# Optimization experiments

Measured on AMD Instinct MI355X. Metric: run time of the kernel, lower is better.

The kernel has to match this reference:

```python
import jax, jax.numpy as jnp
import numpy as np

B, S, D = 2, 2048, 4096
N_Q_HEADS, N_KV_HEADS, HEAD_DIM = 32, 8, 128
N_REP = N_Q_HEADS // N_KV_HEADS
ROPE_THETA = 10000.0


def setup_inputs() -> dict:
    key = jax.random.key(0)
    ks = jax.random.split(key, 5)
    x = jax.random.normal(ks[0], (B, S, D), dtype=jnp.float32)
    sc = 1.0 / np.sqrt(D)
    wq = jax.random.normal(ks[1], (D, N_Q_HEADS * HEAD_DIM), dtype=jnp.float32) * sc
    wk = jax.random.normal(ks[2], (D, N_KV_HEADS * HEAD_DIM), dtype=jnp.float32) * sc
    wv = jax.random.normal(ks[3], (D, N_KV_HEADS * HEAD_DIM), dtype=jnp.float32) * sc
    cache_k = jnp.zeros((B, S, N_KV_HEADS, HEAD_DIM), dtype=jnp.float32)
    cache_v = jnp.zeros((B, S, N_KV_HEADS, HEAD_DIM), dtype=jnp.float32)
    # rotary frequencies: theta_i = 1/ROPE_THETA^(2i/hd), angle = pos * theta_i
    inv_freq = 1.0 / (ROPE_THETA ** (np.arange(0, HEAD_DIM, 2, dtype=np.float32) / HEAD_DIM))
    angles = np.arange(S, dtype=np.float32)[:, None] * inv_freq[None, :]  # [S, hd/2]
    freqs_cos = jnp.asarray(np.cos(angles), dtype=jnp.float32)
    freqs_sin = jnp.asarray(np.sin(angles), dtype=jnp.float32)
    return {"x": x, "wq": wq, "wk": wk, "wv": wv,
            "cache_k": cache_k, "cache_v": cache_v,
            "freqs_cos": freqs_cos, "freqs_sin": freqs_sin,
            "start_pos": 0}


def _apply_rope(x, cos, sin):
    # x: [B, S, H, hd]; cos/sin: [S, hd/2] -> complex rotation of adjacent pairs
    xr = x[..., 0::2]
    xi = x[..., 1::2]
    c = cos[None, :, None, :]
    s = sin[None, :, None, :]
    out_r = xr * c - xi * s
    out_i = xr * s + xi * c
    return jnp.stack([out_r, out_i], axis=-1).reshape(x.shape)


def reference(x, wq, wk, wv, cache_k, cache_v, freqs_cos, freqs_sin, start_pos):
    batch, seq_len, _ = x.shape
    xq = (x @ wq).reshape(batch, seq_len, N_Q_HEADS, HEAD_DIM)
    xk = (x @ wk).reshape(batch, seq_len, N_KV_HEADS, HEAD_DIM)
    xv = (x @ wv).reshape(batch, seq_len, N_KV_HEADS, HEAD_DIM)
    xq = _apply_rope(xq, freqs_cos, freqs_sin)
    xk = _apply_rope(xk, freqs_cos, freqs_sin)
    # KV-cache append
    cache_k = jax.lax.dynamic_update_slice(cache_k, xk, (0, start_pos, 0, 0))
    cache_v = jax.lax.dynamic_update_slice(cache_v, xv, (0, start_pos, 0, 0))
    keys = cache_k[:, : start_pos + seq_len]    # [B, T, Hkv, hd]
    values = cache_v[:, : start_pos + seq_len]
    # GQA: repeat kv heads to match query heads
    keys = jnp.repeat(keys, N_REP, axis=2)      # [B, T, Hq, hd]
    values = jnp.repeat(values, N_REP, axis=2)
    scale = 1.0 / jnp.sqrt(jnp.asarray(HEAD_DIM, dtype=x.dtype))
    scores = jnp.einsum("bqhd,bkhd->bhqk", xq, keys) * scale
    probs = jax.nn.softmax(scores.astype(jnp.float32), axis=-1).astype(xq.dtype)
    out = jnp.einsum("bhqk,bkhd->bqhd", probs, values)
    return out.reshape(batch, seq_len, N_Q_HEADS * HEAD_DIM)
```

## Files before the change

### kernel.cpp

```cpp
#include <hip/hip_runtime.h>

#define BATCH   2
#define S_LEN   2048
#define D_MODEL 4096
#define HD      128
#define NQH     32
#define NKVH    8

typedef unsigned short ushort_t;
typedef __bf16 bf16x8 __attribute__((ext_vector_type(8)));
typedef float floatx4 __attribute__((ext_vector_type(4)));

#define MFMA16(a, b, c) __builtin_amdgcn_mfma_f32_16x16x32_bf16(a, b, c, 0, 0, 0)

#if __has_builtin(__builtin_amdgcn_exp2f)
#define EXP2(x) __builtin_amdgcn_exp2f(x)
#else
#define EXP2(x) __expf((x) * 0.6931471805599453f)
#endif

__device__ __forceinline__ ushort_t f2b(float f) {
    unsigned int x;
    __builtin_memcpy(&x, &f, 4);
    x += 0x7fff + ((x >> 16) & 1);
    return (ushort_t)(x >> 16);
}

__device__ __forceinline__ void gld16(void* lds, const void* g) {
    __builtin_amdgcn_global_load_lds(
        (const __attribute__((address_space(1))) void*)g,
        (__attribute__((address_space(3))) void*)lds, 16, 0, 0);
}

__global__ __launch_bounds__(256) void conv_x(const float* __restrict__ x,
                                              ushort_t* __restrict__ x0,
                                              ushort_t* __restrict__ x1) {
    const size_t i = ((size_t)blockIdx.x * 256 + threadIdx.x) << 2;
    float4 v = *(const float4*)&x[i];
    ushort4 p;
    p.x = f2b(v.x); p.y = f2b(v.y); p.z = f2b(v.z); p.w = f2b(v.w);
    ushort_t* dst = (i < 8388608) ? x0 : x1;
    *(ushort4*)&dst[i & 8388607] = p;
}

__global__ __launch_bounds__(256) void pack_w(const float* __restrict__ wq,
                                              const float* __restrict__ wk,
                                              const float* __restrict__ wv,
                                              ushort_t* __restrict__ WT) {
    __shared__ ushort_t t[64][65];
    const int k0 = blockIdx.x << 6;
    const int n0 = blockIdx.y << 6;
    const float* src;
    int scol, sN;
    if (n0 < 4096)      { src = wq; scol = n0;        sN = 4096; }
    else if (n0 < 5120) { src = wk; scol = n0 - 4096; sN = 1024; }
    else                { src = wv; scol = n0 - 5120; sN = 1024; }
    const int tid = threadIdx.x;
#pragma unroll
    for (int i = 0; i < 16; i++) {
        int idx = tid + (i << 8);
        int r = idx >> 6, c = idx & 63;
        t[r][c] = f2b(src[(size_t)(k0 + r) * sN + scol + c]);
    }
    __syncthreads();
#pragma unroll
    for (int i = 0; i < 16; i++) {
        int idx = tid + (i << 8);
        int r = idx >> 6, c = idx & 63;
        WT[(size_t)(n0 + r) * D_MODEL + k0 + c] = t[c][r];
    }
}

__global__ __launch_bounds__(256) void gemm_qkv(const ushort_t* __restrict__ x0,
                                                const ushort_t* __restrict__ x1,
                                                const ushort_t* __restrict__ WT,
                                                const float* __restrict__ fc,
                                                const float* __restrict__ fs,
                                                ushort_t* __restrict__ Qr,
                                                ushort_t* __restrict__ Kr,
                                                ushort_t* __restrict__ Vt) {
    __shared__ ushort_t At[128 * 64];
    __shared__ ushort_t Bt[128 * 64];
    const int tid  = threadIdx.x;
    const int wid  = tid >> 6;
    const int lane = tid & 63;
    const int bm = blockIdx.y << 7;
    const int bn = blockIdx.x << 7;
    const int wm = (wid & 1) << 6;
    const int wn = (wid >> 1) << 6;

    floatx4 acc[4][4] = {};

    const ushort_t* Xb = (bm < 2048) ? x0 : x1;
    const int bml = bm & 2047;

    const int g = (lane & 7) ^ (lane >> 3);
    const ushort_t* gA = Xb + (size_t)(bml + (wid << 5) + (lane >> 3)) * D_MODEL + (g << 3);
    const ushort_t* gB = WT + (size_t)(bn  + (wid << 5) + (lane >> 3)) * D_MODEL + (g << 3);
    ushort_t* lA = &At[wid << 11];
    ushort_t* lB = &Bt[wid << 11];
    const int l7 = lane & 7;
    const int cl = lane & 15, rg = lane >> 4;

    for (int k0 = 0; k0 < D_MODEL; k0 += 64) {
        __syncthreads();
#pragma unroll
        for (int i = 0; i < 4; i++) {
            gld16(lA + (i << 9), gA + (size_t)(i << 3) * D_MODEL + k0);
            gld16(lB + (i << 9), gB + (size_t)(i << 3) * D_MODEL + k0);
        }
        __syncthreads();
#pragma unroll
        for (int kk = 0; kk < 2; kk++) {
            const int c = (kk << 2) + rg;
            const int slot = (c ^ l7) << 3;
            bf16x8 af[4], bfr[4];
#pragma unroll
            for (int mm = 0; mm < 4; mm++) {
                af[mm]  = *(const bf16x8*)&At[((wm + (mm << 4) + cl) << 6) + slot];
                bfr[mm] = *(const bf16x8*)&Bt[((wn + (mm << 4) + cl) << 6) + slot];
            }
#pragma unroll
            for (int mm = 0; mm < 4; mm++)
#pragma unroll
                for (int nn = 0; nn < 4; nn++)
                    acc[mm][nn] = MFMA16(af[mm], bfr[nn], acc[mm][nn]);
        }
    }

    const int region = blockIdx.x;
    const int b_idx  = bm >> 11;
    const int s0w    = (bm & 2047) + wm;

    if (region < 40) {
        const float oscale = (region < 32)
            ? (0.08838834764831845f * 1.4426950408889634f) : 1.0f;
        ushort_t* dst;
        if (region < 32) dst = Qr + (size_t)(b_idx * NQH  +  region      ) * S_LEN * HD;
        else             dst = Kr + (size_t)(b_idx * NKVH + (region - 32)) * S_LEN * HD;
#pragma unroll
        for (int nn = 0; nn < 4; nn++) {
            const int dcol = wn + (nn << 4) + cl;
            const int d2   = dcol >> 1;
            const float sgn = (dcol & 1) ? 1.0f : -1.0f;
#pragma unroll
            for (int mm = 0; mm < 4; mm++)
#pragma unroll
                for (int r = 0; r < 4; r++) {
                    float v  = acc[mm][nn][r];
                    float pv = __shfl_xor(v, 1);
                    int srow = s0w + (mm << 4) + (rg << 2) + r;
                    float c  = fc[(srow << 6) + d2];
                    float s  = fs[(srow << 6) + d2];
                    float o  = (v * c + sgn * pv * s) * oscale;
                    dst[(size_t)srow * HD + dcol] = f2b(o);
                }
        }
    } else {
        const int kvh = region - 40;
        ushort_t* dst = Vt + (size_t)(b_idx * NKVH + kvh) * HD * S_LEN;
#pragma unroll
        for (int mm = 0; mm < 4; mm++) {
            const int srow = s0w + (mm << 4) + (rg << 2);
#pragma unroll
            for (int nn = 0; nn < 4; nn++) {
                const int dcol = wn + (nn << 4) + cl;
                ushort4 pk;
                pk.x = f2b(acc[mm][nn][0]);
                pk.y = f2b(acc[mm][nn][1]);
                pk.z = f2b(acc[mm][nn][2]);
                pk.w = f2b(acc[mm][nn][3]);
                *(ushort4*)&dst[(size_t)dcol * S_LEN + srow] = pk;
            }
        }
    }
}

__global__ __launch_bounds__(256, 3) void attn(const ushort_t* __restrict__ Qr,
                                               const ushort_t* __restrict__ Kr,
                                               const ushort_t* __restrict__ Vtg,
                                               float* __restrict__ out) {
    __shared__ ushort_t Kt[64 * 128];
    __shared__ ushort_t Vl[128 * 64];
    __shared__ ushort_t Pt[4 * 32 * 68];

    const int tid  = threadIdx.x;
    const int wid  = tid >> 6;
    const int lane = tid & 63;
    const int h  = blockIdx.y;
    const int b  = blockIdx.z;
    const int kh = h >> 2;
    const int q0 = (blockIdx.x << 7) + (wid << 5);

    const int cl = lane & 15, rg = lane >> 4, l7 = lane & 7;

    const ushort_t* Qbase = Qr + ((size_t)(b * NQH + h) * S_LEN + q0 + cl) * HD;
    bf16x8 qf0[4], qf1[4];
#pragma unroll
    for (int dc = 0; dc < 4; dc++) {
        qf0[dc] = *(const bf16x8*)&Qbase[(dc << 5) + (rg << 3)];
        qf1[dc] = *(const bf16x8*)&Qbase[(size_t)16 * HD + (dc << 5) + (rg << 3)];
    }

    floatx4 o0[8] = {}, o1[8] = {};
    float ls0[4] = {0.f, 0.f, 0.f, 0.f};
    float ls1[4] = {0.f, 0.f, 0.f, 0.f};

    const ushort_t* Kb = Kr  + (size_t)(b * NKVH + kh) * S_LEN * HD;
    const ushort_t* Vb = Vtg + (size_t)(b * NKVH + kh) * HD * S_LEN;
    ushort_t* Pw = &Pt[wid * 32 * 68];
    const int gv = (lane & 7) ^ (lane >> 3);

    for (int kt0 = 0; kt0 < S_LEN; kt0 += 64) {
        __syncthreads();
#pragma unroll
        for (int i = 0; i < 4; i++) {
            int issue = (wid << 2) + i;
            int gk = cl ^ (((i & 1) << 2) + rg);
            gld16(&Kt[issue << 9],
                  Kb + (size_t)(kt0 + (issue << 2) + rg) * HD + (gk << 3));
            gld16(&Vl[issue << 9],
                  Vb + (size_t)((issue << 3) + (lane >> 3)) * S_LEN + kt0 + (gv << 3));
        }
        __syncthreads();

        __builtin_amdgcn_s_setprio(1);
#pragma unroll
        for (int kt = 0; kt < 4; kt++) {
            floatx4 a0 = {0.f, 0.f, 0.f, 0.f};
            floatx4 a1 = {0.f, 0.f, 0.f, 0.f};
#pragma unroll
            for (int dc = 0; dc < 4; dc++) {
                int c = (dc << 2) + rg;
                bf16x8 kf = *(const bf16x8*)&Kt[(((kt << 4) + cl) << 7) + ((c ^ l7) << 3)];
                a0 = MFMA16(qf0[dc], kf, a0);
                a1 = MFMA16(qf1[dc], kf, a1);
            }
#pragma unroll
            for (int r = 0; r < 4; r++) {
                float p0 = EXP2(a0[r]);
                float p1 = EXP2(a1[r]);
                ls0[r] += p0;
                ls1[r] += p1;
                Pw[(((rg << 2) + r)     ) * 68 + (kt << 4) + cl] = f2b(p0);
                Pw[(((rg << 2) + r) + 16) * 68 + (kt << 4) + cl] = f2b(p1);
            }
        }

#pragma unroll
        for (int c = 0; c < 2; c++) {
            bf16x8 pf0 = *(const bf16x8*)&Pw[ cl       * 68 + (c << 5) + (rg << 3)];
            bf16x8 pf1 = *(const bf16x8*)&Pw[(cl + 16) * 68 + (c << 5) + (rg << 3)];
#pragma unroll
            for (int dt = 0; dt < 8; dt++) {
                int c2 = (c << 2) + rg;
                bf16x8 vf = *(const bf16x8*)&Vl[(((dt << 4) + cl) << 6) + ((c2 ^ l7) << 3)];
                o0[dt] = MFMA16(pf0, vf, o0[dt]);
                o1[dt] = MFMA16(pf1, vf, o1[dt]);
            }
        }
        __builtin_amdgcn_s_setprio(0);
    }

#pragma unroll
    for (int r = 0; r < 4; r++) {
        float v0 = ls0[r];
        v0 += __shfl_xor(v0, 1);
        v0 += __shfl_xor(v0, 2);
        v0 += __shfl_xor(v0, 4);
        v0 += __shfl_xor(v0, 8);
        ls0[r] = 1.0f / v0;
        float v1 = ls1[r];
        v1 += __shfl_xor(v1, 1);
        v1 += __shfl_xor(v1, 2);
        v1 += __shfl_xor(v1, 4);
        v1 += __shfl_xor(v1, 8);
        ls1[r] = 1.0f / v1;
    }

    float* ob = out + (size_t)(b * S_LEN + q0) * (NQH * HD) + h * HD;
#pragma unroll
    for (int dt = 0; dt < 8; dt++)
#pragma unroll
        for (int r = 0; r < 4; r++) {
            ob[(size_t)((rg << 2) + r) * (NQH * HD) + (dt << 4) + cl] =
                o0[dt][r] * ls0[r];
            ob[(size_t)((rg << 2) + r + 16) * (NQH * HD) + (dt << 4) + cl] =
                o1[dt][r] * ls1[r];
        }
}

extern "C" void kernel_launch(void* const* d_in, const int* in_sizes, int n_in,
                              void* d_out, int out_size, void* d_ws, size_t ws_size,
                              hipStream_t stream) {
    const float* x  = (const float*)d_in[0];
    const float* wq = (const float*)d_in[1];
    const float* wk = (const float*)d_in[2];
    const float* wv = (const float*)d_in[3];
    ushort_t* x0 = (ushort_t*)d_in[4];
    ushort_t* x1 = (ushort_t*)d_in[5];
    const float* fc = (const float*)d_in[6];
    const float* fs = (const float*)d_in[7];
    float* out = (float*)d_out;

    ushort_t* WTx = (ushort_t*)d_in[0];

    char* ws = (char*)d_ws;
    ushort_t* Qr = (ushort_t*)(ws);
    ushort_t* Kr = (ushort_t*)(ws + 33554432);
    ushort_t* Vt = (ushort_t*)(ws + 41943040);

    conv_x  <<<16384,           256, 0, stream>>>(x, x0, x1);
    pack_w  <<<dim3(64, 96),    256, 0, stream>>>(wq, wk, wv, WTx);
    gemm_qkv<<<dim3(48, 32),    256, 0, stream>>>(x0, x1, WTx, fc, fs, Qr, Kr, Vt);
    attn    <<<dim3(16, 32, 2), 256, 0, stream>>>(Qr, Kr, Vt, out);
    (void)in_sizes; (void)n_in; (void)out_size; (void)ws_size;
}
```

Measured before the change: 654.4 us.

## Register-prefetch K/V tiles with padded LDS and smaller KV tile

Replaces direct global-to-LDS loads with XOR swizzle by a register-staged prefetch: the next 32-key K/V tile is loaded into registers while the current tile is computed, then written to padded LDS rows. The KV tile shrinks from 64 to 32 keys, which shrinks LDS use and raises the occupancy hint from 3 to 4 blocks. The aim is to hide global latency and raise occupancy, at the cost of twice as many barriers per sequence and extra VGPRs for the staged data.

```diff
diff --git a/kernel.cpp b/kernel.cpp
--- a/kernel.cpp
+++ b/kernel.cpp
@@ -10,6 +10,7 @@
 typedef unsigned short ushort_t;
 typedef __bf16 bf16x8 __attribute__((ext_vector_type(8)));
 typedef float floatx4 __attribute__((ext_vector_type(4)));
+typedef unsigned short ushortx8 __attribute__((ext_vector_type(8)));
 
 #define MFMA16(a, b, c) __builtin_amdgcn_mfma_f32_16x16x32_bf16(a, b, c, 0, 0, 0)
 
@@ -176,13 +177,17 @@
     }
 }
 
-__global__ __launch_bounds__(256, 3) void attn(const ushort_t* __restrict__ Qr,
+#define KSTR 136
+#define VSTR 40
+#define PSTR 40
+
+__global__ __launch_bounds__(256, 4) void attn(const ushort_t* __restrict__ Qr,
                                                const ushort_t* __restrict__ Kr,
                                                const ushort_t* __restrict__ Vtg,
                                                float* __restrict__ out) {
-    __shared__ ushort_t Kt[64 * 128];
-    __shared__ ushort_t Vl[128 * 64];
-    __shared__ ushort_t Pt[4 * 32 * 68];
+    __shared__ __align__(16) ushort_t Kt[32 * KSTR];
+    __shared__ __align__(16) ushort_t Vl[128 * VSTR];
+    __shared__ __align__(16) ushort_t Pt[4 * 32 * PSTR];
 
     const int tid  = threadIdx.x;
     const int wid  = tid >> 6;
@@ -192,7 +197,7 @@
     const int kh = h >> 2;
     const int q0 = (blockIdx.x << 7) + (wid << 5);
 
-    const int cl = lane & 15, rg = lane >> 4, l7 = lane & 7;
+    const int cl = lane & 15, rg = lane >> 4;
 
     const ushort_t* Qbase = Qr + ((size_t)(b * NQH + h) * S_LEN + q0 + cl) * HD;
     bf16x8 qf0[4], qf1[4];
@@ -208,31 +213,59 @@
 
     const ushort_t* Kb = Kr  + (size_t)(b * NKVH + kh) * S_LEN * HD;
     const ushort_t* Vb = Vtg + (size_t)(b * NKVH + kh) * HD * S_LEN;
-    ushort_t* Pw = &Pt[wid * 32 * 68];
-    const int gv = (lane & 7) ^ (lane >> 3);
-
-    for (int kt0 = 0; kt0 < S_LEN; kt0 += 64) {
-        __syncthreads();
-#pragma unroll
-        for (int i = 0; i < 4; i++) {
-            int issue = (wid << 2) + i;
-            int gk = cl ^ (((i & 1) << 2) + rg);
-            gld16(&Kt[issue << 9],
-                  Kb + (size_t)(kt0 + (issue << 2) + rg) * HD + (gk << 3));
-            gld16(&Vl[issue << 9],
-                  Vb + (size_t)((issue << 3) + (lane >> 3)) * S_LEN + kt0 + (gv << 3));
-        }
-        __syncthreads();
+    ushort_t* Pw = &Pt[wid * 32 * PSTR];
+
+    const int krow = tid >> 3;
+    const int kcol = (tid & 7) << 4;
+    const int vrow = tid >> 1;
+    const int vcol = (tid & 1) << 4;
+    const ushort_t* gK = Kb + (size_t)krow * HD + kcol;
+    const ushort_t* gV = Vb + (size_t)vrow * S_LEN + vcol;
+
+    ushortx8 ka, kb2, va, vb2;
+    {
+        const ushort_t* p = gK;
+        ka  = *(const ushortx8*)(p);
+        kb2 = *(const ushortx8*)(p + 8);
+        const ushort_t* q = gV;
+        va  = *(const ushortx8*)(q);
+        vb2 = *(const ushortx8*)(q + 8);
+    }
+
+#pragma unroll 1
+    for (int t = 0; t < 64; t++) {
+        asm volatile("" ::: "memory");
+        __builtin_amdgcn_s_barrier();
+        asm volatile("" ::: "memory");
+
+        *(ushortx8*)&Kt[krow * KSTR + kcol]     = ka;
+        *(ushortx8*)&Kt[krow * KSTR + kcol + 8] = kb2;
+        *(ushortx8*)&Vl[vrow * VSTR + vcol]     = va;
+        *(ushortx8*)&Vl[vrow * VSTR + vcol + 8] = vb2;
+
+        if (t < 63) {
+            const int kt0 = (t + 1) << 5;
+            const ushort_t* p = gK + (size_t)kt0 * HD;
+            ka  = *(const ushortx8*)(p);
+            kb2 = *(const ushortx8*)(p + 8);
+            const ushort_t* q = gV + kt0;
+            va  = *(const ushortx8*)(q);
+            vb2 = *(const ushortx8*)(q + 8);
+        }
+
+        asm volatile("s_waitcnt lgkmcnt(0)" ::: "memory");
+        __builtin_amdgcn_s_barrier();
+        asm volatile("" ::: "memory");
 
         __builtin_amdgcn_s_setprio(1);
 #pragma unroll
-        for (int kt = 0; kt < 4; kt++) {
+        for (int kt = 0; kt < 2; kt++) {
             floatx4 a0 = {0.f, 0.f, 0.f, 0.f};
             floatx4 a1 = {0.f, 0.f, 0.f, 0.f};
 #pragma unroll
             for (int dc = 0; dc < 4; dc++) {
-                int c = (dc << 2) + rg;
-                bf16x8 kf = *(const bf16x8*)&Kt[(((kt << 4) + cl) << 7) + ((c ^ l7) << 3)];
+                bf16x8 kf = *(const bf16x8*)
+                    &Kt[((kt << 4) + cl) * KSTR + (((dc << 2) + rg) << 3)];
                 a0 = MFMA16(qf0[dc], kf, a0);
                 a1 = MFMA16(qf1[dc], kf, a1);
             }
@@ -242,19 +275,18 @@
                 float p1 = EXP2(a1[r]);
                 ls0[r] += p0;
                 ls1[r] += p1;
-                Pw[(((rg << 2) + r)     ) * 68 + (kt << 4) + cl] = f2b(p0);
-                Pw[(((rg << 2) + r) + 16) * 68 + (kt << 4) + cl] = f2b(p1);
-            }
-        }
-
-#pragma unroll
-        for (int c = 0; c < 2; c++) {
-            bf16x8 pf0 = *(const bf16x8*)&Pw[ cl       * 68 + (c << 5) + (rg << 3)];
-            bf16x8 pf1 = *(const bf16x8*)&Pw[(cl + 16) * 68 + (c << 5) + (rg << 3)];
+                Pw[(((rg << 2) + r)     ) * PSTR + (kt << 4) + cl] = f2b(p0);
+                Pw[(((rg << 2) + r) + 16) * PSTR + (kt << 4) + cl] = f2b(p1);
+            }
+        }
+
+        {
+            bf16x8 pf0 = *(const bf16x8*)&Pw[ cl       * PSTR + (rg << 3)];
+            bf16x8 pf1 = *(const bf16x8*)&Pw[(cl + 16) * PSTR + (rg << 3)];
 #pragma unroll
             for (int dt = 0; dt < 8; dt++) {
-                int c2 = (c << 2) + rg;
-                bf16x8 vf = *(const bf16x8*)&Vl[(((dt << 4) + cl) << 6) + ((c2 ^ l7) << 3)];
+                bf16x8 vf = *(const bf16x8*)
+                    &Vl[((dt << 4) + cl) * VSTR + (rg << 3)];
                 o0[dt] = MFMA16(pf0, vf, o0[dt]);
                 o1[dt] = MFMA16(pf1, vf, o1[dt]);
             }
```

Measured after the change: 874.2 us. 33.6% more time.

## Double-buffer K/V tiles in attention with 32-key steps and async prefetch

Applied to the files above, without the earlier changes.

The attention loop moves from single-buffered 64-key tiles to double-buffered 32-key tiles. The next tile's global-to-LDS loads are issued before computing on the current one, with explicit vmcnt waits and raw barriers, so load latency can overlap with MFMA work. The cost is more iterations and barriers per key range and a reworked swizzle for the smaller V tile, though LDS use stays about the same.

```diff
diff --git a/kernel.cpp b/kernel.cpp
--- a/kernel.cpp
+++ b/kernel.cpp
@@ -180,9 +180,9 @@
                                                const ushort_t* __restrict__ Kr,
                                                const ushort_t* __restrict__ Vtg,
                                                float* __restrict__ out) {
-    __shared__ ushort_t Kt[64 * 128];
-    __shared__ ushort_t Vl[128 * 64];
-    __shared__ ushort_t Pt[4 * 32 * 68];
+    __shared__ ushort_t Ktb[2][32 * 128];
+    __shared__ ushort_t Vlb[2][128 * 32];
+    __shared__ ushort_t Pt[4 * 32 * 40];
 
     const int tid  = threadIdx.x;
     const int wid  = tid >> 6;
@@ -208,31 +208,49 @@
 
     const ushort_t* Kb = Kr  + (size_t)(b * NKVH + kh) * S_LEN * HD;
     const ushort_t* Vb = Vtg + (size_t)(b * NKVH + kh) * HD * S_LEN;
-    ushort_t* Pw = &Pt[wid * 32 * 68];
-    const int gv = (lane & 7) ^ (lane >> 3);
-
-    for (int kt0 = 0; kt0 < S_LEN; kt0 += 64) {
-        __syncthreads();
-#pragma unroll
-        for (int i = 0; i < 4; i++) {
-            int issue = (wid << 2) + i;
-            int gk = cl ^ (((i & 1) << 2) + rg);
-            gld16(&Kt[issue << 9],
-                  Kb + (size_t)(kt0 + (issue << 2) + rg) * HD + (gk << 3));
-            gld16(&Vl[issue << 9],
-                  Vb + (size_t)((issue << 3) + (lane >> 3)) * S_LEN + kt0 + (gv << 3));
-        }
-        __syncthreads();
+    ushort_t* Pw = &Pt[wid * 32 * 40];
+
+    const int vr  = lane >> 2;
+    const int gv2 = (lane & 3) ^ (vr & 3);
+
+    auto stage = [&](int bi, int kt0) {
+#pragma unroll
+        for (int i = 0; i < 2; i++) {
+            int ki = (wid << 1) + i;
+            gld16(&Ktb[bi][ki << 9],
+                  Kb + (size_t)(kt0 + (ki << 2) + rg) * HD
+                     + ((cl ^ (((ki & 1) << 2) + rg)) << 3));
+            gld16(&Vlb[bi][ki << 9],
+                  Vb + (size_t)((ki << 4) + vr) * S_LEN + kt0 + (gv2 << 3));
+        }
+    };
+
+    stage(0, 0);
+
+#pragma unroll 1
+    for (int t = 0; t < 64; t++) {
+        if (t < 63) {
+            stage((t + 1) & 1, (t + 1) << 5);
+            asm volatile("s_waitcnt vmcnt(4)" ::: "memory");
+        } else {
+            asm volatile("s_waitcnt vmcnt(0)" ::: "memory");
+        }
+        __builtin_amdgcn_s_barrier();
+        asm volatile("" ::: "memory");
+
+        const ushort_t* Kc = Ktb[t & 1];
+        const ushort_t* Vc = Vlb[t & 1];
 
         __builtin_amdgcn_s_setprio(1);
 #pragma unroll
-        for (int kt = 0; kt < 4; kt++) {
+        for (int kt = 0; kt < 2; kt++) {
             floatx4 a0 = {0.f, 0.f, 0.f, 0.f};
             floatx4 a1 = {0.f, 0.f, 0.f, 0.f};
 #pragma unroll
             for (int dc = 0; dc < 4; dc++) {
                 int c = (dc << 2) + rg;
-                bf16x8 kf = *(const bf16x8*)&Kt[(((kt << 4) + cl) << 7) + ((c ^ l7) << 3)];
+                bf16x8 kf = *(const bf16x8*)
+                    &Kc[(((kt << 4) + cl) << 7) + ((c ^ l7) << 3)];
                 a0 = MFMA16(qf0[dc], kf, a0);
                 a1 = MFMA16(qf1[dc], kf, a1);
             }
@@ -242,24 +260,27 @@
                 float p1 = EXP2(a1[r]);
                 ls0[r] += p0;
                 ls1[r] += p1;
-                Pw[(((rg << 2) + r)     ) * 68 + (kt << 4) + cl] = f2b(p0);
-                Pw[(((rg << 2) + r) + 16) * 68 + (kt << 4) + cl] = f2b(p1);
-            }
-        }
-
-#pragma unroll
-        for (int c = 0; c < 2; c++) {
-            bf16x8 pf0 = *(const bf16x8*)&Pw[ cl       * 68 + (c << 5) + (rg << 3)];
-            bf16x8 pf1 = *(const bf16x8*)&Pw[(cl + 16) * 68 + (c << 5) + (rg << 3)];
+                Pw[(((rg << 2) + r)     ) * 40 + (kt << 4) + cl] = f2b(p0);
+                Pw[(((rg << 2) + r) + 16) * 40 + (kt << 4) + cl] = f2b(p1);
+            }
+        }
+
+        {
+            bf16x8 pf0 = *(const bf16x8*)&Pw[ cl       * 40 + (rg << 3)];
+            bf16x8 pf1 = *(const bf16x8*)&Pw[(cl + 16) * 40 + (rg << 3)];
 #pragma unroll
             for (int dt = 0; dt < 8; dt++) {
-                int c2 = (c << 2) + rg;
-                bf16x8 vf = *(const bf16x8*)&Vl[(((dt << 4) + cl) << 6) + ((c2 ^ l7) << 3)];
+                int d = (dt << 4) + cl;
+                bf16x8 vf = *(const bf16x8*)
+                    &Vc[(d << 5) + ((rg ^ (cl & 3)) << 3)];
                 o0[dt] = MFMA16(pf0, vf, o0[dt]);
                 o1[dt] = MFMA16(pf1, vf, o1[dt]);
             }
         }
         __builtin_amdgcn_s_setprio(0);
+
+        asm volatile("" ::: "memory");
+        __builtin_amdgcn_s_barrier();
     }
 
 #pragma unroll
```

Result: faster. 614.8 us (-6.1%).
